# Kernel optimization log

Measured on AMD Instinct MI355X. Metric: run time of the kernel, lower is better.

The kernel has to match this reference:

```python
import jax, jax.numpy as jnp
import numpy as np

D_MODEL = 2048
DOWN = 512
UP = 1024
NUM_HEADS = 16
ROPE_DIM = 64
BS = 16
SEQ = 512
BASE = 10000.0
HEAD_DIM = D_MODEL // NUM_HEADS          # 128 (used only in the softmax scale)
V_HEAD_DIM = UP // NUM_HEADS             # 64


def _linear(x, W, b):
    # torch nn.Linear: y = x @ W.T + b, W shape (out, in)
    return x @ W.T + b


def _rope(x, num_heads, rope_dim):
    # Faithful to source RotaryEmbedding, including the swapped sin/cos caches:
    #   cos_pos = sin(pos*theta), sin_pos = cos(pos*theta)
    bs, L, _ = x.shape
    q = x.reshape(bs, L, num_heads, rope_dim).transpose(0, 2, 1, 3)  # (bs,h,L,d)
    theta = 1.0 / (BASE ** (jnp.arange(0, rope_dim, 2, dtype=jnp.float32) / rope_dim))
    ang = jnp.arange(L, dtype=jnp.float32)[:, None] * theta[None, :]   # (L, d/2)
    cos_pos = jnp.repeat(jnp.sin(ang), 2, axis=-1)  # (L, d) -- source quirk
    sin_pos = jnp.repeat(jnp.cos(ang), 2, axis=-1)
    q2 = jnp.stack([-q[..., 1::2], q[..., ::2]], axis=-1).reshape(bs, num_heads, L, rope_dim)
    return q * cos_pos + q2 * sin_pos


def setup_inputs() -> dict:
    key = jax.random.key(0)
    ks = jax.random.split(key, 18)
    s = 0.02
    d = {
        "h": jax.random.normal(ks[0], (BS, SEQ, D_MODEL), jnp.float32),
        "W_down_kv": jax.random.normal(ks[1], (DOWN, D_MODEL), jnp.float32) * s,
        "b_down_kv": jnp.zeros((DOWN,), jnp.float32),
        "W_up_k": jax.random.normal(ks[2], (UP, DOWN), jnp.float32) * s,
        "b_up_k": jnp.zeros((UP,), jnp.float32),
        "W_up_v": jax.random.normal(ks[3], (UP, DOWN), jnp.float32) * s,
        "b_up_v": jnp.zeros((UP,), jnp.float32),
        "W_down_q": jax.random.normal(ks[4], (DOWN, D_MODEL), jnp.float32) * s,
        "b_down_q": jnp.zeros((DOWN,), jnp.float32),
        "W_up_q": jax.random.normal(ks[5], (UP, DOWN), jnp.float32) * s,
        "b_up_q": jnp.zeros((UP,), jnp.float32),
        "W_qr": jax.random.normal(ks[6], (ROPE_DIM * NUM_HEADS, DOWN), jnp.float32) * s,
        "b_qr": jnp.zeros((ROPE_DIM * NUM_HEADS,), jnp.float32),
        "W_kr": jax.random.normal(ks[7], (ROPE_DIM, D_MODEL), jnp.float32) * s,
        "b_kr": jnp.zeros((ROPE_DIM,), jnp.float32),
        "W_fc": jax.random.normal(ks[8], (D_MODEL, NUM_HEADS * V_HEAD_DIM), jnp.float32) * s,
        "b_fc": jnp.zeros((D_MODEL,), jnp.float32),
    }
    return d


def reference(h, W_down_kv, b_down_kv, W_up_k, b_up_k, W_up_v, b_up_v,
              W_down_q, b_down_q, W_up_q, b_up_q, W_qr, b_qr,
              W_kr, b_kr, W_fc, b_fc):
    bs, L, _ = h.shape
    # low-rank KV path
    c_kv = _linear(h, W_down_kv, b_down_kv)             # (bs,L,down)
    k_c = _linear(c_kv, W_up_k, b_up_k)                 # (bs,L,up)
    v_c = _linear(c_kv, W_up_v, b_up_v)                 # (bs,L,up)
    # low-rank Q path
    c_q = _linear(h, W_down_q, b_down_q)                # (bs,L,down)
    q_c = _linear(c_q, W_up_q, b_up_q)                  # (bs,L,up)
    # rope (decoupled) path
    q_r = _rope(_linear(c_q, W_qr, b_qr), NUM_HEADS, ROPE_DIM)  # (bs,H,L,rope)
    k_r = _rope(_linear(h, W_kr, b_kr), 1, ROPE_DIM)            # (bs,1,L,rope)

    q_c = q_c.reshape(bs, L, NUM_HEADS, -1).transpose(0, 2, 1, 3)  # (bs,H,L,64)
    q = jnp.concatenate([q_c, q_r], axis=-1)                        # (bs,H,L,128)
    k_c = k_c.reshape(bs, L, NUM_HEADS, -1).transpose(0, 2, 1, 3)
    k_r = jnp.broadcast_to(k_r, (bs, NUM_HEADS, L, ROPE_DIM))       # shared across heads
    k = jnp.concatenate([k_c, k_r], axis=-1)

    scale = 1.0 / jnp.sqrt(jnp.float32(HEAD_DIM + ROPE_DIM))  # sqrt(192), per source
    scores = jnp.einsum('bhqd,bhkd->bhqk', q, k) * scale
    attn = jax.nn.softmax(scores, axis=-1)  # dropout is identity in eval mode

    v = v_c.reshape(bs, L, NUM_HEADS, V_HEAD_DIM).transpose(0, 2, 1, 3)
    out = jnp.einsum('bhqk,bhkd->bhqd', attn, v)
    out = out.transpose(0, 2, 1, 3).reshape(bs, L, -1)   # (bs,L,H*v_head_dim)
    return _linear(out, W_fc, b_fc)                      # (bs,L,d_model)
```

## Files before the change

### kernel.cpp

```cpp
#include <hip/hip_runtime.h>
#include <hip/hip_bf16.h>

typedef __bf16 bf16x8 __attribute__((ext_vector_type(8)));
typedef float f32x4 __attribute__((ext_vector_type(4)));
using u16 = unsigned short;
using u32 = unsigned int;

__device__ __forceinline__ float bf2f(u16 v) {
    unsigned int u = (unsigned int)v << 16;
    float f; __builtin_memcpy(&f, &u, 4); return f;
}
__device__ __forceinline__ u16 f2bf(float f) {
    unsigned int u; __builtin_memcpy(&u, &f, 4);
    u += 0x7FFFu + ((u >> 16) & 1u);
    return (u16)(u >> 16);
}

struct Cvt9 {
    const float* src[9];
    u16* dst[9];
    int end[9];
};
__global__ __launch_bounds__(256) void cvt_all(Cvt9 d, int total)
{
    int c = blockIdx.x * 256 + threadIdx.x;
    if (c >= total) return;
    int seg = 0;
    while (c >= d.end[seg]) ++seg;
    int local = c - (seg ? d.end[seg - 1] : 0);
    const float* s = d.src[seg] + (size_t)local * 8;
    float4 f0 = *(const float4*)s;
    float4 f1 = *(const float4*)(s + 4);
    u16 tmp[8] = { f2bf(f0.x), f2bf(f0.y), f2bf(f0.z), f2bf(f0.w),
                   f2bf(f1.x), f2bf(f1.y), f2bf(f1.z), f2bf(f1.w) };
    *(uint4*)(d.dst[seg] + (size_t)local * 8) = *(const uint4*)tmp;
}

struct Cpy7 {
    const float* src[7];
    float* dst[7];
    int end[7];
};
__global__ __launch_bounds__(256) void copy_f32(Cpy7 d, int total)
{
    int c = blockIdx.x * 256 + threadIdx.x;
    if (c >= total) return;
    int seg = 0;
    while (c >= d.end[seg]) ++seg;
    int local = c - (seg ? d.end[seg - 1] : 0);
    d.dst[seg][local] = d.src[seg][local];
}

template<bool CF>
__global__ __launch_bounds__(256) void gemm_v4(
    const u16* __restrict__ A0, const u16* __restrict__ B0, void* __restrict__ C0, const float* __restrict__ e0,
    const u16* __restrict__ A1, const u16* __restrict__ B1, void* __restrict__ C1, const float* __restrict__ e1,
    int ysplit, int lda, int ldb, int ldc, int N, int K)
{
    __shared__ __align__(16) u16 As[2][128 * 32];
    __shared__ __align__(16) u16 Bs[2][128 * 32];

    const int t = threadIdx.x;
    const int lane = t & 63;
    const int w = t >> 6;
    const int wm = w >> 1, wn = w & 1;
    const int l16 = lane & 15, quad = lane >> 4;
    const int m0 = blockIdx.x * 128;

    const u16* A; const u16* B; void* Cv; const float* bias; int yl;
    if ((int)blockIdx.y < ysplit) { A = A0; B = B0; Cv = C0; bias = e0; yl = blockIdx.y; }
    else                          { A = A1; B = B1; Cv = C1; bias = e1; yl = blockIdx.y - ysplit; }
    const int n0 = yl * 128;

    const int sub  = lane >> 2;
    const int slot = lane & 3;
    const int agc  = slot ^ ((sub >> 1) & 3);
    const int sfr  = (l16 >> 1) & 3;

    f32x4 acc[4][4];
#pragma unroll
    for (int i = 0; i < 4; ++i)
#pragma unroll
        for (int j = 0; j < 4; ++j) acc[i][j] = (f32x4){0.f, 0.f, 0.f, 0.f};

    auto STAGE = [&](int buf, int k0) {
#pragma unroll
        for (int c = 0; c < 2; ++c) {
            const int rr = w * 32 + c * 16;
            const u16* ga = A + (size_t)(m0 + rr + sub) * lda + k0 + agc * 8;
            __builtin_amdgcn_global_load_lds(
                (const __attribute__((address_space(1))) u32*)ga,
                (__attribute__((address_space(3))) u32*)&As[buf][rr * 32], 16, 0, 0);
            const u16* gb = B + (size_t)(n0 + rr + sub) * ldb + k0 + agc * 8;
            __builtin_amdgcn_global_load_lds(
                (const __attribute__((address_space(1))) u32*)gb,
                (__attribute__((address_space(3))) u32*)&Bs[buf][rr * 32], 16, 0, 0);
        }
    };

    const int nt = K >> 5;
    STAGE(0, 0);
    for (int tt = 0; tt < nt; ++tt) {
        const int cur = tt & 1;
        if (tt + 1 < nt) {
            STAGE(cur ^ 1, (tt + 1) << 5);
            asm volatile("s_waitcnt vmcnt(4)");
        } else {
            asm volatile("s_waitcnt vmcnt(0)");
        }
        __builtin_amdgcn_sched_barrier(0);
        __builtin_amdgcn_s_barrier();
        __builtin_amdgcn_sched_barrier(0);

        const u16* Ab = As[cur];
        const u16* Bb = Bs[cur];
        bf16x8 af[4], bfr[4];
#pragma unroll
        for (int i = 0; i < 4; ++i)
            af[i] = *(const bf16x8*)&Ab[(wm * 64 + i * 16 + l16) * 32 + (quad ^ sfr) * 8];
#pragma unroll
        for (int j = 0; j < 4; ++j)
            bfr[j] = *(const bf16x8*)&Bb[(wn * 64 + j * 16 + l16) * 32 + (quad ^ sfr) * 8];
#pragma unroll
        for (int i = 0; i < 4; ++i)
#pragma unroll
            for (int j = 0; j < 4; ++j)
                acc[i][j] = __builtin_amdgcn_mfma_f32_16x16x32_bf16(af[i], bfr[j], acc[i][j], 0, 0, 0);

        __builtin_amdgcn_s_barrier();
        __builtin_amdgcn_sched_barrier(0);
    }

#pragma unroll
    for (int j = 0; j < 4; ++j) {
        int col = n0 + wn * 64 + j * 16 + l16;
        if (col >= N) continue;
        float bv = bias[col];
#pragma unroll
        for (int i = 0; i < 4; ++i) {
#pragma unroll
            for (int r = 0; r < 4; ++r) {
                int row = m0 + wm * 64 + i * 16 + quad * 4 + r;
                float v = acc[i][j][r] + bv;
                if (CF) ((float*)Cv)[(size_t)row * ldc + col] = v;
                else    ((u16*)Cv)[(size_t)row * ldc + col] = f2bf(v);
            }
        }
    }
}

__global__ void rope_inplace(u16* __restrict__ buf, int ld, int col0, int ppr, int total)
{
    int idx = blockIdx.x * 256 + threadIdx.x;
    if (idx >= total) return;
    int row = idx / ppr;
    int pi  = idx - row * ppr;
    int grp = pi >> 5;
    int i   = pi & 31;
    int pos = row & 511;
    float theta = __expf(-(float)i * 0.2878231366242558f);
    float ang = (float)pos * theta;
    float s = sinf(ang), c = cosf(ang);
    size_t base = (size_t)row * ld + col0 + grp * 64 + 2 * i;
    float x0 = bf2f(buf[base]);
    float x1 = bf2f(buf[base + 1]);
    buf[base]     = f2bf(x0 * s - x1 * c);
    buf[base + 1] = f2bf(x1 * s + x0 * c);
}

__global__ __launch_bounds__(256) void attn_kernel(
    const u16* __restrict__ q_src,
    const u16* __restrict__ kv_src,
    const u16* __restrict__ kr_src,
    u16* __restrict__ o_dst, int ldo)
{
    __shared__ __align__(16) u16 Ks[64 * 136];
    __shared__ __align__(16) u16 Vt[64 * 72];
    __shared__ __align__(16) u16 Ps[64 * 72];

    const int t = threadIdx.x;
    const int lane = t & 63;
    const int w = t >> 6;
    const int l16 = lane & 15, quad = lane >> 4;

    const int id   = blockIdx.x;
    const int xcd  = id & 7;
    const int qt   = (id >> 3) & 7;
    const int panel = xcd + ((id >> 6) << 3);
    const int h = panel & 15;
    const int b = panel >> 4;
    const int qrow0 = b * 512 + qt * 64;
    const int krow_base = b * 512;

    bf16x8 aq[4];
    {
        const u16* qrow = q_src + (size_t)(qrow0 + w * 16 + l16) * 2048;
#pragma unroll
        for (int ks = 0; ks < 4; ++ks) {
            int col = ks * 32 + quad * 8;
            const u16* src = (col < 64) ? qrow + h * 64 + col
                                        : qrow + 1024 + h * 64 + (col - 64);
            aq[ks] = *(const bf16x8*)src;
        }
    }

    const int colK = (t & 15) * 8;
    const int r0k  = t >> 4;
    const u16* kbase; int kstr;
    if (colK < 64) { kbase = kv_src + h * 64 + colK;        kstr = 2048; }
    else           { kbase = kr_src + 1024 + (colK - 64);   kstr = 1088; }
    u16* kw = &Ks[r0k * 136 + colK];

    const int v00 = (t & 7) * 8;
    const int r0v = t >> 3;
    const u16* vbase = kv_src + 1024 + h * 64 + v00;
    const int rotA = (r0v + v00) & 63;
    const int rotB = (r0v + 32 + v00) & 63;
    u16* vwA = &Vt[v00 * 72 + rotA];
    u16* vwB = &Vt[v00 * 72 + rotB];

    auto LOADT = [&](int krow0, uint4& K0, uint4& K1, uint4& K2, uint4& K3,
                     uint4& V0, uint4& V1) {
        K0 = *(const uint4*)(kbase + (size_t)(krow0 + r0k     ) * kstr);
        K1 = *(const uint4*)(kbase + (size_t)(krow0 + r0k + 16) * kstr);
        K2 = *(const uint4*)(kbase + (size_t)(krow0 + r0k + 32) * kstr);
        K3 = *(const uint4*)(kbase + (size_t)(krow0 + r0k + 48) * kstr);
        V0 = *(const uint4*)(vbase + (size_t)(krow0 + r0v     ) * 2048);
        V1 = *(const uint4*)(vbase + (size_t)(krow0 + r0v + 32) * 2048);
    };
    auto WRITET = [&](const uint4& K0, const uint4& K1, const uint4& K2, const uint4& K3,
                      const uint4& V0, const uint4& V1) {
        *(uint4*)(kw)            = K0;
        *(uint4*)(kw + 16 * 136) = K1;
        *(uint4*)(kw + 32 * 136) = K2;
        *(uint4*)(kw + 48 * 136) = K3;
        u16 ta[8], tb[8];
        __builtin_memcpy(ta, &V0, 16);
        __builtin_memcpy(tb, &V1, 16);
#pragma unroll
        for (int j2 = 0; j2 < 8; ++j2) { vwA[j2 * 72] = ta[j2]; vwB[j2 * 72] = tb[j2]; }
    };

    float m2[4], l_run[4];
    f32x4 o[4];
#pragma unroll
    for (int r = 0; r < 4; ++r) { m2[r] = -1e30f; l_run[r] = 0.f; }
#pragma unroll
    for (int n = 0; n < 4; ++n) o[n] = (f32x4){0.f, 0.f, 0.f, 0.f};

    const float C = 0.10411756f;
    const int Rp = (64 - (quad << 4)) & 48;
    const int Rr = (64 - ((l16 >> 2) << 4)) & 48;

    uint4 kA0, kA1, kA2, kA3, vA0, vA1;
    uint4 kB0, kB1, kB2, kB3, vB0, vB1;
    LOADT(krow_base, kA0, kA1, kA2, kA3, vA0, vA1);

    for (int kt = 0; kt < 8; ++kt) {
        __builtin_amdgcn_s_barrier();
        __builtin_amdgcn_sched_barrier(0);
        if ((kt & 1) == 0) {
            WRITET(kA0, kA1, kA2, kA3, vA0, vA1);
            if (kt < 7) LOADT(krow_base + (kt + 1) * 64, kB0, kB1, kB2, kB3, vB0, vB1);
        } else {
            WRITET(kB0, kB1, kB2, kB3, vB0, vB1);
            if (kt < 7) LOADT(krow_base + (kt + 1) * 64, kA0, kA1, kA2, kA3, vA0, vA1);
        }
        asm volatile("s_waitcnt lgkmcnt(0)");
        __builtin_amdgcn_sched_barrier(0);
        __builtin_amdgcn_s_barrier();
        __builtin_amdgcn_sched_barrier(0);

        f32x4 s[4];
#pragma unroll
        for (int n = 0; n < 4; ++n) s[n] = (f32x4){0.f, 0.f, 0.f, 0.f};
#pragma unroll
        for (int ks = 0; ks < 4; ++ks) {
#pragma unroll
            for (int n = 0; n < 4; ++n) {
                bf16x8 bk = *(const bf16x8*)&Ks[(n * 16 + l16) * 136 + ks * 32 + quad * 8];
                s[n] = __builtin_amdgcn_mfma_f32_16x16x32_bf16(aq[ks], bk, s[n], 0, 0, 0);
            }
        }

        float mx[4], alpha[4], rs[4];
#pragma unroll
        for (int r = 0; r < 4; ++r)
            mx[r] = fmaxf(fmaxf(s[0][r], s[1][r]), fmaxf(s[2][r], s[3][r]));
#pragma unroll
        for (int d = 1; d < 16; d <<= 1)
#pragma unroll
            for (int r = 0; r < 4; ++r)
                mx[r] = fmaxf(mx[r], __shfl_xor(mx[r], d));
#pragma unroll
        for (int r = 0; r < 4; ++r) {
            float mnew = fmaxf(m2[r], mx[r] * C);
            alpha[r] = __builtin_amdgcn_exp2f(m2[r] - mnew);
            m2[r] = mnew;
            rs[r] = 0.f;
#pragma unroll
            for (int n = 0; n < 4; ++n) {
                float pv = __builtin_amdgcn_exp2f(__builtin_fmaf(s[n][r], C, -mnew));
                s[n][r] = pv;
                rs[r] += pv;
            }
        }
#pragma unroll
        for (int d = 1; d < 16; d <<= 1)
#pragma unroll
            for (int r = 0; r < 4; ++r)
                rs[r] += __shfl_xor(rs[r], d);
#pragma unroll
        for (int r = 0; r < 4; ++r) {
            l_run[r] = l_run[r] * alpha[r] + rs[r];
#pragma unroll
            for (int n = 0; n < 4; ++n) o[n][r] *= alpha[r];
        }

#pragma unroll
        for (int n = 0; n < 4; ++n) {
            int pc = (n * 16 + l16 + Rp) & 63;
#pragma unroll
            for (int r = 0; r < 4; ++r)
                Ps[(w * 16 + quad * 4 + r) * 72 + pc] = f2bf(s[n][r]);
        }

#pragma unroll
        for (int kk = 0; kk < 2; ++kk) {
            bf16x8 ap = *(const bf16x8*)&Ps[(w * 16 + l16) * 72 + ((kk * 32 + quad * 8 + Rr) & 63)];
#pragma unroll
            for (int n = 0; n < 4; ++n) {
                bf16x8 bv = *(const bf16x8*)&Vt[(n * 16 + l16) * 72
                              + ((kk * 32 + quad * 8 + n * 16 + (l16 & 8)) & 63)];
                o[n] = __builtin_amdgcn_mfma_f32_16x16x32_bf16(ap, bv, o[n], 0, 0, 0);
            }
        }
    }

#pragma unroll
    for (int r = 0; r < 4; ++r) {
        float inv = 1.0f / l_run[r];
        int row = qrow0 + w * 16 + quad * 4 + r;
#pragma unroll
        for (int n = 0; n < 4; ++n) {
            int col = h * 64 + n * 16 + l16;
            o_dst[(size_t)row * ldo + col] = f2bf(o[n][r] * inv);
        }
    }
}

extern "C" void kernel_launch(void* const* d_in, const int* in_sizes, int n_in,
                              void* d_out, int out_size, void* d_ws, size_t ws_size,
                              hipStream_t stream)
{
    const float* h    = (const float*)d_in[0];
    const float* Wdkv = (const float*)d_in[1];
    const float* bdkv = (const float*)d_in[2];
    const float* Wuk  = (const float*)d_in[3];
    const float* buk  = (const float*)d_in[4];
    const float* Wuv  = (const float*)d_in[5];
    const float* buv  = (const float*)d_in[6];
    const float* Wdq  = (const float*)d_in[7];
    const float* bdq  = (const float*)d_in[8];
    const float* Wuq  = (const float*)d_in[9];
    const float* buq  = (const float*)d_in[10];
    const float* Wqr  = (const float*)d_in[11];
    const float* bqr  = (const float*)d_in[12];
    const float* Wkr  = (const float*)d_in[13];
    const float* bkr  = (const float*)d_in[14];
    const float* Wfc  = (const float*)d_in[15];
    const float* bfc  = (const float*)d_in[16];

    char* ws = (char*)d_ws;
    u16* out1   = (u16*)ws;
    u16* hbf    = (u16*)(ws + 17825792);
    u16* out2a  = hbf;
    u16* out2b  = (u16*)(ws + 51380224);
    u16* w1     = (u16*)(ws + 84934656);
    u16* w2a    = (u16*)(ws + 89653248);
    u16* w2b    = (u16*)(ws + 91750400);
    u16* wfc    = (u16*)(ws + 93847552);
    float* bias_s1 = (float*)(ws + 98041856);
    float* bias_2  = (float*)(ws + 98046208);

    Cvt9 cd;
    const float* srcs[9] = { h, Wdkv, Wdq, Wkr, Wuk, Wuv, Wuq, Wqr, Wfc };
    u16* dsts[9] = { hbf, w1, w1 + 512 * 2048, w1 + 1024 * 2048,
                     w2a, w2a + 1024 * 512, w2b, w2b + 1024 * 512, wfc };
    int cnts[9] = { 2097152, 131072, 131072, 16384, 65536, 65536, 65536, 65536, 262144 };
    int acc2 = 0;
    for (int i = 0; i < 9; ++i) { cd.src[i] = srcs[i]; cd.dst[i] = dsts[i]; acc2 += cnts[i]; cd.end[i] = acc2; }
    cvt_all<<<(acc2 + 255) / 256, 256, 0, stream>>>(cd, acc2);
    hipMemsetAsync(w1 + 1088 * 2048, 0, 64 * 2048 * sizeof(u16), stream);

    Cpy7 bc;
    const float* bs[7] = { bdkv, bdq, bkr, buk, buv, buq, bqr };
    float* bd[7] = { bias_s1, bias_s1 + 512, bias_s1 + 1024,
                     bias_2, bias_2 + 1024, bias_2 + 2048, bias_2 + 3072 };
    int bn[7] = { 512, 512, 64, 1024, 1024, 1024, 1024 };
    int bacc = 0;
    for (int i = 0; i < 7; ++i) { bc.src[i] = bs[i]; bc.dst[i] = bd[i]; bacc += bn[i]; bc.end[i] = bacc; }
    copy_f32<<<(bacc + 255) / 256, 256, 0, stream>>>(bc, bacc);

    gemm_v4<false><<<dim3(64, 9), 256, 0, stream>>>(
        hbf, w1, out1, bias_s1,
        hbf, w1, out1, bias_s1, 9, 2048, 2048, 1088, 1088, 2048);
    rope_inplace<<<1024, 256, 0, stream>>>(out1, 1088, 1024, 32, 8192 * 32);

    gemm_v4<false><<<dim3(64, 32), 256, 0, stream>>>(
        out1,       w2a, out2a, bias_2,
        out1 + 512, w2b, out2b, bias_2 + 2048, 16, 1088, 512, 2048, 2048, 512);
    rope_inplace<<<16384, 256, 0, stream>>>(out2b, 2048, 1024, 512, 8192 * 512);

    attn_kernel<<<2048, 256, 0, stream>>>(out2b, out2a, out1, out1, 1088);

    gemm_v4<true><<<dim3(64, 16), 256, 0, stream>>>(
        out1, wfc, d_out, bfc,
        out1, wfc, d_out, bfc, 16, 1088, 1024, 2048, 2048, 1024);
}
```

Measured before the change: 431.1 us.

## Triple-buffer GEMM LDS staging and vectorize epilogue via swapped MFMA operands

```diff
diff --git a/kernel.cpp b/kernel.cpp
--- a/kernel.cpp
+++ b/kernel.cpp
@@ -52,13 +52,13 @@
 }
 
 template<bool CF>
-__global__ __launch_bounds__(256) void gemm_v4(
+__global__ __launch_bounds__(256) void gemm_v5(
     const u16* __restrict__ A0, const u16* __restrict__ B0, void* __restrict__ C0, const float* __restrict__ e0,
     const u16* __restrict__ A1, const u16* __restrict__ B1, void* __restrict__ C1, const float* __restrict__ e1,
     int ysplit, int lda, int ldb, int ldc, int N, int K)
 {
-    __shared__ __align__(16) u16 As[2][128 * 32];
-    __shared__ __align__(16) u16 Bs[2][128 * 32];
+    __shared__ __align__(16) u16 As[3][128 * 32];
+    __shared__ __align__(16) u16 Bs[3][128 * 32];
 
     const int t = threadIdx.x;
     const int lane = t & 63;
@@ -100,10 +100,14 @@
 
     const int nt = K >> 5;
     STAGE(0, 0);
+    STAGE(1, 32);
+    int cur = 0;
     for (int tt = 0; tt < nt; ++tt) {
-        const int cur = tt & 1;
-        if (tt + 1 < nt) {
-            STAGE(cur ^ 1, (tt + 1) << 5);
+        int pre = cur + 2; if (pre >= 3) pre -= 3;
+        if (tt + 2 < nt) {
+            STAGE(pre, (tt + 2) << 5);
+            asm volatile("s_waitcnt vmcnt(8)");
+        } else if (tt + 1 < nt) {
             asm volatile("s_waitcnt vmcnt(4)");
         } else {
             asm volatile("s_waitcnt vmcnt(0)");
@@ -125,25 +129,31 @@
         for (int i = 0; i < 4; ++i)
 #pragma unroll
             for (int j = 0; j < 4; ++j)
-                acc[i][j] = __builtin_amdgcn_mfma_f32_16x16x32_bf16(af[i], bfr[j], acc[i][j], 0, 0, 0);
+                acc[i][j] = __builtin_amdgcn_mfma_f32_16x16x32_bf16(bfr[j], af[i], acc[i][j], 0, 0, 0);
 
         __builtin_amdgcn_s_barrier();
         __builtin_amdgcn_sched_barrier(0);
+        cur += 1; if (cur >= 3) cur -= 3;
     }
 
 #pragma unroll
-    for (int j = 0; j < 4; ++j) {
-        int col = n0 + wn * 64 + j * 16 + l16;
-        if (col >= N) continue;
-        float bv = bias[col];
-#pragma unroll
-        for (int i = 0; i < 4; ++i) {
-#pragma unroll
-            for (int r = 0; r < 4; ++r) {
-                int row = m0 + wm * 64 + i * 16 + quad * 4 + r;
-                float v = acc[i][j][r] + bv;
-                if (CF) ((float*)Cv)[(size_t)row * ldc + col] = v;
-                else    ((u16*)Cv)[(size_t)row * ldc + col] = f2bf(v);
+    for (int i = 0; i < 4; ++i) {
+        const int row = m0 + wm * 64 + i * 16 + l16;
+#pragma unroll
+        for (int j = 0; j < 4; ++j) {
+            const int colb = n0 + wn * 64 + j * 16 + quad * 4;
+            if (colb >= N) continue;
+            float4 bv = *(const float4*)&bias[colb];
+            float v0 = acc[i][j][0] + bv.x;
+            float v1 = acc[i][j][1] + bv.y;
+            float v2 = acc[i][j][2] + bv.z;
+            float v3 = acc[i][j][3] + bv.w;
+            if (CF) {
+                float4 out = { v0, v1, v2, v3 };
+                *(float4*)((float*)Cv + (size_t)row * ldc + colb) = out;
+            } else {
+                u16 p[4] = { f2bf(v0), f2bf(v1), f2bf(v2), f2bf(v3) };
+                *(uint2*)((u16*)Cv + (size_t)row * ldc + colb) = *(const uint2*)p;
             }
         }
     }
@@ -402,19 +412,19 @@
     for (int i = 0; i < 7; ++i) { bc.src[i] = bs[i]; bc.dst[i] = bd[i]; bacc += bn[i]; bc.end[i] = bacc; }
     copy_f32<<<(bacc + 255) / 256, 256, 0, stream>>>(bc, bacc);
 
-    gemm_v4<false><<<dim3(64, 9), 256, 0, stream>>>(
+    gemm_v5<false><<<dim3(64, 9), 256, 0, stream>>>(
         hbf, w1, out1, bias_s1,
         hbf, w1, out1, bias_s1, 9, 2048, 2048, 1088, 1088, 2048);
     rope_inplace<<<1024, 256, 0, stream>>>(out1, 1088, 1024, 32, 8192 * 32);
 
-    gemm_v4<false><<<dim3(64, 32), 256, 0, stream>>>(
+    gemm_v5<false><<<dim3(64, 32), 256, 0, stream>>>(
         out1,       w2a, out2a, bias_2,
         out1 + 512, w2b, out2b, bias_2 + 2048, 16, 1088, 512, 2048, 2048, 512);
     rope_inplace<<<16384, 256, 0, stream>>>(out2b, 2048, 1024, 512, 8192 * 512);
 
     attn_kernel<<<2048, 256, 0, stream>>>(out2b, out2a, out1, out1, 1088);
 
-    gemm_v4<true><<<dim3(64, 16), 256, 0, stream>>>(
+    gemm_v5<true><<<dim3(64, 16), 256, 0, stream>>>(
         out1, wfc, d_out, bfc,
         out1, wfc, d_out, bfc, 16, 1088, 1024, 2048, 2048, 1024);
 }
```

Result: no change. 434.9 us (+0.9%).
